# Kernel tuning notes

Measured on AMD Instinct MI355X. Metric: run time of the kernel, lower is better.

## Reference

```python
import jax, jax.numpy as jnp
import numpy as np

T, I, H, L = 2048, 64, 512, 5  # seq len, input feat, hidden, layers


def _lstm_layer(x_seq, w_ih, w_hh, b_ih, b_hh):
    """Single-layer LSTM over time, batch=1. x_seq: [T, in]. Returns [T, H]."""
    n_hidden = w_hh.shape[1]
    b = b_ih + b_hh  # fuse biases once

    def step(carry, x_t):
        h, c = carry
        gates = w_ih @ x_t + w_hh @ h + b  # [4H]
        i, f, g, o = jnp.split(gates, 4)
        i = jax.nn.sigmoid(i)
        f = jax.nn.sigmoid(f)
        g = jnp.tanh(g)
        o = jax.nn.sigmoid(o)
        c = f * c + i * g
        h = o * jnp.tanh(c)
        return (h, c), h

    h0 = jnp.zeros((n_hidden,), x_seq.dtype)
    (_, _), hs = jax.lax.scan(step, (h0, h0), x_seq)
    return hs


def setup_inputs() -> dict:
    key = jax.random.key(0)
    ks = jax.random.split(key, 12)
    s = 1.0 / np.sqrt(H)  # PyTorch-style U(-1/sqrt(H), 1/sqrt(H)) scale, approximated with scaled normal
    return {
        "x": jax.random.normal(ks[0], (T, I), jnp.float32),
        "w_ih0": jax.random.normal(ks[1], (4 * H, I), jnp.float32) * s,
        "w_hh0": jax.random.normal(ks[2], (4 * H, H), jnp.float32) * s,
        "b_ih0": jax.random.normal(ks[3], (4 * H,), jnp.float32) * s,
        "b_hh0": jax.random.normal(ks[4], (4 * H,), jnp.float32) * s,
        "w_ih": jax.random.normal(ks[5], (L - 1, 4 * H, H), jnp.float32) * s,
        "w_hh": jax.random.normal(ks[6], (L - 1, 4 * H, H), jnp.float32) * s,
        "b_ih": jax.random.normal(ks[7], (L - 1, 4 * H), jnp.float32) * s,
        "b_hh": jax.random.normal(ks[8], (L - 1, 4 * H), jnp.float32) * s,
        "w_lin": jax.random.normal(ks[9], (1, H), jnp.float32) * s,
        "b_lin": jax.random.normal(ks[10], (1,), jnp.float32) * s,
    }


def reference(x, w_ih0, w_hh0, b_ih0, b_hh0, w_ih, w_hh, b_ih, b_hh, w_lin, b_lin):
    # 5-layer LSTM (dropout=0 / inference), batch = 1
    h = _lstm_layer(x, w_ih0, w_hh0, b_ih0, b_hh0)  # [T, H]
    for l in range(w_ih.shape[0]):  # fixed small layer loop
        h = _lstm_layer(h, w_ih[l], w_hh[l], b_ih[l], b_hh[l])
    e = h @ w_lin.T + b_lin                # [T, 1]
    w = jax.nn.softmax(jnp.tanh(e), axis=0)  # softmax over time
    res = jnp.mean(h * w, axis=0, keepdims=True)  # [1, H] (matches torch (T,1,H)*(T,1) mean over axis 0)
    return res
```

## Files before the change

kernel.cpp:

```cpp
#include <hip/hip_runtime.h>
#include <math.h>

#define TT 2048
#define II 64
#define HH 512
#define LL 5
#define RING 8
#define BPL 32
#define NBLK (LL * BPL)
#define WPB 16

__device__ __forceinline__ float wave_sum(float v) {
#pragma unroll
  for (int m = 32; m > 0; m >>= 1) v += __shfl_xor(v, m, 64);
  return v;
}

__device__ __forceinline__ float wave_max(float v) {
#pragma unroll
  for (int m = 32; m > 0; m >>= 1) v = fmaxf(v, __shfl_xor(v, m, 64));
  return v;
}

__device__ __forceinline__ float sigmoidf_(float v) {
  return 1.0f / (1.0f + expf(-v));
}

__device__ __forceinline__ unsigned ld_cnt(const unsigned* p) {
  return __hip_atomic_load((unsigned*)p, __ATOMIC_RELAXED, __HIP_MEMORY_SCOPE_AGENT);
}

__device__ __forceinline__ void wait_ge(unsigned* p, unsigned v) {
  long spins = 0;
  while (ld_cnt(p) < v) {
    if (++spins > 8000000L) {
      __hip_atomic_fetch_max(p, v, __ATOMIC_RELAXED, __HIP_MEMORY_SCOPE_AGENT);
      break;
    }
  }
}

__device__ __forceinline__ float ld_coh(const float* p) {
  return __hip_atomic_load((float*)p, __ATOMIC_RELAXED, __HIP_MEMORY_SCOPE_AGENT);
}
__device__ __forceinline__ void st_coh(float* p, float v) {
  __hip_atomic_store(p, v, __ATOMIC_RELAXED, __HIP_MEMORY_SCOPE_AGENT);
}

__device__ __forceinline__ void grid_barrier(unsigned* arrive, unsigned* gen, unsigned idx) {
  __syncthreads();
  if (threadIdx.x == 0) {
    __threadfence();
    unsigned target = (unsigned)NBLK * (idx + 1u);
    unsigned prev = __hip_atomic_fetch_add(arrive, 1u, __ATOMIC_RELAXED, __HIP_MEMORY_SCOPE_AGENT);
    if (prev + 1u == target) {
      __hip_atomic_store(gen, idx + 1u, __ATOMIC_RELAXED, __HIP_MEMORY_SCOPE_AGENT);
    } else {
      wait_ge(gen, idx + 1u);
    }
    __threadfence();
  }
  __syncthreads();
}

extern "C" __global__ void __launch_bounds__(1024, 4) lstm_pipe(
    const float* __restrict__ x,
    const float* __restrict__ w_ih0, const float* __restrict__ w_hh0,
    const float* __restrict__ b_ih0, const float* __restrict__ b_hh0,
    const float* __restrict__ w_ih, const float* __restrict__ w_hh,
    const float* __restrict__ b_ih, const float* __restrict__ b_hh,
    const float* __restrict__ w_lin, const float* __restrict__ b_lin,
    float* __restrict__ out, float* __restrict__ ws) {
  unsigned* cnt = (unsigned*)ws;
  float* data = ws + 1024;
  float* h_ring = data;
  float* h4 = h_ring + LL * RING * HH;
  float* h4T = h4 + (size_t)TT * HH;
  float* scores = h4T + (size_t)HH * TT;
  float* pbuf = scores + TT;
  float* red = pbuf + TT;

  const int b = blockIdx.x;
  const int tid = threadIdx.x;
  const int wv = tid >> 6;
  const int lane = tid & 63;
  const int l = b / BPL;
  const int q = b % BPL;
  const int j = q * WPB + wv;

  unsigned* arr_l = cnt + l * 64;
  unsigned* arr_lm1 = cnt + (l - 1) * 64;
  unsigned* arr_lp1 = cnt + (l + 1) * 64;
  unsigned* garr = cnt + 320;
  unsigned* ggen = cnt + 336;

  float whh[4][8], wih[4][8], bias[4];
  const float* WHH = (l == 0) ? w_hh0 : (w_hh + (size_t)(l - 1) * 4 * HH * HH);
#pragma unroll
  for (int g = 0; g < 4; ++g) {
    const int row = g * HH + j;
#pragma unroll
    for (int m = 0; m < 8; ++m) whh[g][m] = WHH[(size_t)row * HH + m * 64 + lane];
  }
  if (l == 0) {
#pragma unroll
    for (int g = 0; g < 4; ++g) {
      const int row = g * HH + j;
      wih[g][0] = w_ih0[(size_t)row * II + lane];
#pragma unroll
      for (int m = 1; m < 8; ++m) wih[g][m] = 0.0f;
      bias[g] = b_ih0[row] + b_hh0[row];
    }
  } else {
    const float* WIH = w_ih + (size_t)(l - 1) * 4 * HH * HH;
    const float* BIH = b_ih + (size_t)(l - 1) * 4 * HH;
    const float* BHH = b_hh + (size_t)(l - 1) * 4 * HH;
#pragma unroll
    for (int g = 0; g < 4; ++g) {
      const int row = g * HH + j;
#pragma unroll
      for (int m = 0; m < 8; ++m) wih[g][m] = WIH[(size_t)row * HH + m * 64 + lane];
      bias[g] = BIH[row] + BHH[row];
    }
  }
#pragma unroll
  for (int g = 0; g < 4; ++g) {
#pragma unroll
    for (int m = 0; m < 8; ++m) {
      asm volatile("" : "+v"(whh[g][m]));
      asm volatile("" : "+v"(wih[g][m]));
    }
    asm volatile("" : "+v"(bias[g]));
  }

  const float* own_rd = h_ring + (size_t)l * RING * HH + lane;
  const float* prev_rd = h_ring + (size_t)(l - 1) * RING * HH + lane;
  float* own_wr = h_ring + (size_t)l * RING * HH + j;

  float c = 0.0f;

  for (int t = 0; t < TT; ++t) {
    if (tid == 0 && t > 0) wait_ge(arr_l, (unsigned)(BPL * t));
    if (tid == 64 && l > 0) wait_ge(arr_lm1, (unsigned)(BPL * (t + 1)));
    if (tid == 128 && l < LL - 1 && t >= RING)
      wait_ge(arr_lp1, (unsigned)(BPL * (t - RING + 1)));
    __syncthreads();

    float hp[8];
    if (t > 0) {
      const float* rp = own_rd + (size_t)((t - 1) & (RING - 1)) * HH;
#pragma unroll
      for (int m = 0; m < 8; ++m) hp[m] = ld_coh(rp + m * 64);
    } else {
#pragma unroll
      for (int m = 0; m < 8; ++m) hp[m] = 0.0f;
    }
    float xin[8];
    if (l == 0) {
      xin[0] = x[(size_t)t * II + lane];
#pragma unroll
      for (int m = 1; m < 8; ++m) xin[m] = 0.0f;
    } else {
      const float* rp = prev_rd + (size_t)(t & (RING - 1)) * HH;
#pragma unroll
      for (int m = 0; m < 8; ++m) xin[m] = ld_coh(rp + m * 64);
    }

    float ai = 0.0f, af = 0.0f, ag = 0.0f, ao = 0.0f;
#pragma unroll
    for (int m = 0; m < 8; ++m) {
      ai = fmaf(whh[0][m], hp[m], ai);
      af = fmaf(whh[1][m], hp[m], af);
      ag = fmaf(whh[2][m], hp[m], ag);
      ao = fmaf(whh[3][m], hp[m], ao);
    }
#pragma unroll
    for (int m = 0; m < 8; ++m) {
      ai = fmaf(wih[0][m], xin[m], ai);
      af = fmaf(wih[1][m], xin[m], af);
      ag = fmaf(wih[2][m], xin[m], ag);
      ao = fmaf(wih[3][m], xin[m], ao);
    }
    ai = wave_sum(ai); af = wave_sum(af); ag = wave_sum(ag); ao = wave_sum(ao);
    float gi = sigmoidf_(ai + bias[0]);
    float gf = sigmoidf_(af + bias[1]);
    float gg = tanhf(ag + bias[2]);
    float go = sigmoidf_(ao + bias[3]);
    c = gf * c + gi * gg;
    float h = go * tanhf(c);
    if (lane == 0) {
      st_coh(own_wr + (size_t)(t & (RING - 1)) * HH, h);
      if (l == LL - 1) {
        h4[(size_t)t * HH + j] = h;
        h4T[(size_t)j * TT + t] = h;
      }
    }
    asm volatile("s_waitcnt vmcnt(0)" ::: "memory");
    __syncthreads();
    if (tid == 0) {
      __hip_atomic_fetch_add(arr_l, 1u, __ATOMIC_RELAXED, __HIP_MEMORY_SCOPE_AGENT);
    }
  }

  grid_barrier(garr, ggen, 0u);

  {
    const int gw = b * WPB + wv;
    if (gw < TT) {
      const int t = gw;
      const float4* hp4 = (const float4*)(h4 + (size_t)t * HH + lane * 8);
      const float4* wl4 = (const float4*)(w_lin + lane * 8);
      float4 a = hp4[0], d = hp4[1], wa = wl4[0], wd = wl4[1];
      float acc = 0.0f;
      acc = fmaf(a.x, wa.x, acc); acc = fmaf(a.y, wa.y, acc);
      acc = fmaf(a.z, wa.z, acc); acc = fmaf(a.w, wa.w, acc);
      acc = fmaf(d.x, wd.x, acc); acc = fmaf(d.y, wd.y, acc);
      acc = fmaf(d.z, wd.z, acc); acc = fmaf(d.w, wd.w, acc);
      acc = wave_sum(acc);
      float sc = tanhf(acc + b_lin[0]);
      if (lane == 0) scores[t] = sc;
    }
  }
  grid_barrier(garr, ggen, 1u);

  __shared__ float sbuf[20];
  if (b == 0) {
    float s0 = scores[tid];
    float s1 = scores[tid + 1024];
    float m = fmaxf(s0, s1);
    m = wave_max(m);
    if (lane == 0) sbuf[wv] = m;
    __syncthreads();
    if (tid == 0) {
      float M = sbuf[0];
      for (int k = 1; k < 16; ++k) M = fmaxf(M, sbuf[k]);
      sbuf[16] = M;
    }
    __syncthreads();
    float M = sbuf[16];
    float p0 = expf(s0 - M), p1 = expf(s1 - M);
    pbuf[tid] = p0;
    pbuf[tid + 1024] = p1;
    float ssum = wave_sum(p0 + p1);
    __syncthreads();
    if (lane == 0) sbuf[wv] = ssum;
    __syncthreads();
    if (tid == 0) {
      float S = 0.0f;
      for (int k = 0; k < 16; ++k) S += sbuf[k];
      red[0] = 1.0f / ((float)TT * S);
    }
  }
  grid_barrier(garr, ggen, 2u);

  {
    const int gw = b * WPB + wv;
    if (gw < HH) {
      const int jj = gw;
      const float scale = red[0];
      const float* hr = h4T + (size_t)jj * TT + lane * 32;
      const float* pr = pbuf + lane * 32;
      float acc = 0.0f;
#pragma unroll
      for (int m = 0; m < 32; ++m) acc = fmaf(hr[m], pr[m], acc);
      acc = wave_sum(acc);
      if (lane == 0) out[jj] = scale * acc;
    }
  }
}

extern "C" void kernel_launch(void* const* d_in, const int* in_sizes, int n_in,
                              void* d_out, int out_size, void* d_ws, size_t ws_size,
                              hipStream_t stream) {
  hipMemsetAsync(d_ws, 0, 4096, stream);
  lstm_pipe<<<dim3(NBLK), dim3(1024), 0, stream>>>(
      (const float*)d_in[0],
      (const float*)d_in[1], (const float*)d_in[2],
      (const float*)d_in[3], (const float*)d_in[4],
      (const float*)d_in[5], (const float*)d_in[6],
      (const float*)d_in[7], (const float*)d_in[8],
      (const float*)d_in[9], (const float*)d_in[10],
      (float*)d_out, (float*)d_ws);
}
```

Measured before the change: 8.911 ms.

## Replace per-step counters with tagged ring entries polled by each wave

```diff
diff --git a/kernel.cpp b/kernel.cpp
--- a/kernel.cpp
+++ b/kernel.cpp
@@ -8,7 +8,10 @@
 #define RING 8
 #define BPL 32
 #define NBLK (LL * BPL)
-#define WPB 16
+#define WPB 8
+#define JPW 2
+
+typedef unsigned long long u64;
 
 __device__ __forceinline__ float wave_sum(float v) {
 #pragma unroll
@@ -26,25 +29,24 @@
   return 1.0f / (1.0f + expf(-v));
 }
 
-__device__ __forceinline__ unsigned ld_cnt(const unsigned* p) {
+__device__ __forceinline__ u64 ld8(const u64* p) {
+  return __hip_atomic_load((u64*)p, __ATOMIC_RELAXED, __HIP_MEMORY_SCOPE_AGENT);
+}
+__device__ __forceinline__ void st8(u64* p, u64 v) {
+  __hip_atomic_store(p, v, __ATOMIC_RELAXED, __HIP_MEMORY_SCOPE_AGENT);
+}
+__device__ __forceinline__ unsigned ld4(const unsigned* p) {
   return __hip_atomic_load((unsigned*)p, __ATOMIC_RELAXED, __HIP_MEMORY_SCOPE_AGENT);
 }
 
 __device__ __forceinline__ void wait_ge(unsigned* p, unsigned v) {
   long spins = 0;
-  while (ld_cnt(p) < v) {
+  while (ld4(p) < v) {
     if (++spins > 8000000L) {
       __hip_atomic_fetch_max(p, v, __ATOMIC_RELAXED, __HIP_MEMORY_SCOPE_AGENT);
       break;
     }
   }
-}
-
-__device__ __forceinline__ float ld_coh(const float* p) {
-  return __hip_atomic_load((float*)p, __ATOMIC_RELAXED, __HIP_MEMORY_SCOPE_AGENT);
-}
-__device__ __forceinline__ void st_coh(float* p, float v) {
-  __hip_atomic_store(p, v, __ATOMIC_RELAXED, __HIP_MEMORY_SCOPE_AGENT);
 }
 
 __device__ __forceinline__ void grid_barrier(unsigned* arrive, unsigned* gen, unsigned idx) {
@@ -63,7 +65,7 @@
   __syncthreads();
 }
 
-extern "C" __global__ void __launch_bounds__(1024, 4) lstm_pipe(
+extern "C" __global__ void __launch_bounds__(512, 2) lstm_pipe(
     const float* __restrict__ x,
     const float* __restrict__ w_ih0, const float* __restrict__ w_hh0,
     const float* __restrict__ b_ih0, const float* __restrict__ b_hh0,
@@ -72,9 +74,8 @@
     const float* __restrict__ w_lin, const float* __restrict__ b_lin,
     float* __restrict__ out, float* __restrict__ ws) {
   unsigned* cnt = (unsigned*)ws;
-  float* data = ws + 1024;
-  float* h_ring = data;
-  float* h4 = h_ring + LL * RING * HH;
+  u64* ring = (u64*)(ws + 1024);
+  float* h4 = (float*)(ring + (size_t)LL * RING * HH);
   float* h4T = h4 + (size_t)TT * HH;
   float* scores = h4T + (size_t)HH * TT;
   float* pbuf = scores + TT;
@@ -86,168 +87,211 @@
   const int lane = tid & 63;
   const int l = b / BPL;
   const int q = b % BPL;
-  const int j = q * WPB + wv;
-
-  unsigned* arr_l = cnt + l * 64;
-  unsigned* arr_lm1 = cnt + (l - 1) * 64;
-  unsigned* arr_lp1 = cnt + (l + 1) * 64;
+  const int j0 = (q * WPB + wv) * JPW;
+
+  unsigned* prog_l = cnt + l * 64;
+  unsigned* prog_lp1 = cnt + (l + 1) * 64;
   unsigned* garr = cnt + 320;
   unsigned* ggen = cnt + 336;
 
-  float whh[4][8], wih[4][8], bias[4];
+  float whh[JPW][4][8], wih[JPW][4][8], bias[JPW][4];
   const float* WHH = (l == 0) ? w_hh0 : (w_hh + (size_t)(l - 1) * 4 * HH * HH);
 #pragma unroll
-  for (int g = 0; g < 4; ++g) {
-    const int row = g * HH + j;
-#pragma unroll
-    for (int m = 0; m < 8; ++m) whh[g][m] = WHH[(size_t)row * HH + m * 64 + lane];
+  for (int jj = 0; jj < JPW; ++jj) {
+#pragma unroll
+    for (int g = 0; g < 4; ++g) {
+      const int row = g * HH + j0 + jj;
+#pragma unroll
+      for (int m = 0; m < 8; ++m) whh[jj][g][m] = WHH[(size_t)row * HH + m * 64 + lane];
+    }
   }
   if (l == 0) {
 #pragma unroll
-    for (int g = 0; g < 4; ++g) {
-      const int row = g * HH + j;
-      wih[g][0] = w_ih0[(size_t)row * II + lane];
-#pragma unroll
-      for (int m = 1; m < 8; ++m) wih[g][m] = 0.0f;
-      bias[g] = b_ih0[row] + b_hh0[row];
+    for (int jj = 0; jj < JPW; ++jj) {
+#pragma unroll
+      for (int g = 0; g < 4; ++g) {
+        const int row = g * HH + j0 + jj;
+        wih[jj][g][0] = w_ih0[(size_t)row * II + lane];
+#pragma unroll
+        for (int m = 1; m < 8; ++m) wih[jj][g][m] = 0.0f;
+        bias[jj][g] = b_ih0[row] + b_hh0[row];
+      }
     }
   } else {
     const float* WIH = w_ih + (size_t)(l - 1) * 4 * HH * HH;
     const float* BIH = b_ih + (size_t)(l - 1) * 4 * HH;
     const float* BHH = b_hh + (size_t)(l - 1) * 4 * HH;
 #pragma unroll
-    for (int g = 0; g < 4; ++g) {
-      const int row = g * HH + j;
-#pragma unroll
-      for (int m = 0; m < 8; ++m) wih[g][m] = WIH[(size_t)row * HH + m * 64 + lane];
-      bias[g] = BIH[row] + BHH[row];
-    }
-  }
-#pragma unroll
-  for (int g = 0; g < 4; ++g) {
-#pragma unroll
-    for (int m = 0; m < 8; ++m) {
-      asm volatile("" : "+v"(whh[g][m]));
-      asm volatile("" : "+v"(wih[g][m]));
-    }
-    asm volatile("" : "+v"(bias[g]));
-  }
-
-  const float* own_rd = h_ring + (size_t)l * RING * HH + lane;
-  const float* prev_rd = h_ring + (size_t)(l - 1) * RING * HH + lane;
-  float* own_wr = h_ring + (size_t)l * RING * HH + j;
-
-  float c = 0.0f;
+    for (int jj = 0; jj < JPW; ++jj) {
+#pragma unroll
+      for (int g = 0; g < 4; ++g) {
+        const int row = g * HH + j0 + jj;
+#pragma unroll
+        for (int m = 0; m < 8; ++m) wih[jj][g][m] = WIH[(size_t)row * HH + m * 64 + lane];
+        bias[jj][g] = BIH[row] + BHH[row];
+      }
+    }
+  }
+
+  u64* ringL = ring + (size_t)l * RING * HH;
+  u64* ringP = ring + (size_t)(l - 1) * RING * HH;
+
+  float cst[JPW];
+#pragma unroll
+  for (int jj = 0; jj < JPW; ++jj) cst[jj] = 0.0f;
+
+  const bool need_prev = (l > 0);
+  const bool is_last = (l == LL - 1);
 
   for (int t = 0; t < TT; ++t) {
-    if (tid == 0 && t > 0) wait_ge(arr_l, (unsigned)(BPL * t));
-    if (tid == 64 && l > 0) wait_ge(arr_lm1, (unsigned)(BPL * (t + 1)));
-    if (tid == 128 && l < LL - 1 && t >= RING)
-      wait_ge(arr_lp1, (unsigned)(BPL * (t - RING + 1)));
-    __syncthreads();
-
-    float hp[8];
-    if (t > 0) {
-      const float* rp = own_rd + (size_t)((t - 1) & (RING - 1)) * HH;
-#pragma unroll
-      for (int m = 0; m < 8; ++m) hp[m] = ld_coh(rp + m * 64);
-    } else {
-#pragma unroll
-      for (int m = 0; m < 8; ++m) hp[m] = 0.0f;
-    }
-    float xin[8];
+    const int so = (t - 1) & (RING - 1);
+    const int sp = t & (RING - 1);
+    const u64* own_rd = ringL + (size_t)so * HH + lane;
+    const u64* prev_rd = ringP + (size_t)sp * HH + lane;
+    const bool need_own = (t > 0);
+    const bool need_bp = (l < LL - 1) && (t >= RING);
+    const unsigned bp_min = (unsigned)(t - (RING - 2));
+
+    u64 po[8], pp[8];
+    long spins = 0;
+    for (;;) {
+      if (need_own) {
+#pragma unroll
+        for (int m = 0; m < 8; ++m) po[m] = ld8(own_rd + m * 64);
+      }
+      if (need_prev) {
+#pragma unroll
+        for (int m = 0; m < 8; ++m) pp[m] = ld8(prev_rd + m * 64);
+      }
+      unsigned pg = need_bp ? ld4(prog_lp1) : 0xFFFFFFFFu;
+      bool ok = true;
+      if (need_own) {
+#pragma unroll
+        for (int m = 0; m < 8; ++m) ok &= ((unsigned)(po[m] >> 32) == (unsigned)t);
+      }
+      if (need_prev) {
+#pragma unroll
+        for (int m = 0; m < 8; ++m) ok &= ((unsigned)(pp[m] >> 32) == (unsigned)(t + 1));
+      }
+      if (need_bp) ok &= (pg >= bp_min);
+      if (__ballot(ok) == ~0ull) break;
+      if (++spins > 4000000L) break;
+    }
+
+    float hp[8], xin[8];
+#pragma unroll
+    for (int m = 0; m < 8; ++m) hp[m] = need_own ? __uint_as_float((unsigned)po[m]) : 0.0f;
     if (l == 0) {
       xin[0] = x[(size_t)t * II + lane];
 #pragma unroll
       for (int m = 1; m < 8; ++m) xin[m] = 0.0f;
     } else {
-      const float* rp = prev_rd + (size_t)(t & (RING - 1)) * HH;
-#pragma unroll
-      for (int m = 0; m < 8; ++m) xin[m] = ld_coh(rp + m * 64);
-    }
-
-    float ai = 0.0f, af = 0.0f, ag = 0.0f, ao = 0.0f;
+#pragma unroll
+      for (int m = 0; m < 8; ++m) xin[m] = __uint_as_float((unsigned)pp[m]);
+    }
+
+    float acc[JPW][4];
+#pragma unroll
+    for (int jj = 0; jj < JPW; ++jj)
+#pragma unroll
+      for (int g = 0; g < 4; ++g) acc[jj][g] = 0.0f;
 #pragma unroll
     for (int m = 0; m < 8; ++m) {
-      ai = fmaf(whh[0][m], hp[m], ai);
-      af = fmaf(whh[1][m], hp[m], af);
-      ag = fmaf(whh[2][m], hp[m], ag);
-      ao = fmaf(whh[3][m], hp[m], ao);
+      const float hv = hp[m];
+#pragma unroll
+      for (int jj = 0; jj < JPW; ++jj) {
+        acc[jj][0] = fmaf(whh[jj][0][m], hv, acc[jj][0]);
+        acc[jj][1] = fmaf(whh[jj][1][m], hv, acc[jj][1]);
+        acc[jj][2] = fmaf(whh[jj][2][m], hv, acc[jj][2]);
+        acc[jj][3] = fmaf(whh[jj][3][m], hv, acc[jj][3]);
+      }
     }
 #pragma unroll
     for (int m = 0; m < 8; ++m) {
-      ai = fmaf(wih[0][m], xin[m], ai);
-      af = fmaf(wih[1][m], xin[m], af);
-      ag = fmaf(wih[2][m], xin[m], ag);
-      ao = fmaf(wih[3][m], xin[m], ao);
-    }
-    ai = wave_sum(ai); af = wave_sum(af); ag = wave_sum(ag); ao = wave_sum(ao);
-    float gi = sigmoidf_(ai + bias[0]);
-    float gf = sigmoidf_(af + bias[1]);
-    float gg = tanhf(ag + bias[2]);
-    float go = sigmoidf_(ao + bias[3]);
-    c = gf * c + gi * gg;
-    float h = go * tanhf(c);
+      const float xv = xin[m];
+#pragma unroll
+      for (int jj = 0; jj < JPW; ++jj) {
+        acc[jj][0] = fmaf(wih[jj][0][m], xv, acc[jj][0]);
+        acc[jj][1] = fmaf(wih[jj][1][m], xv, acc[jj][1]);
+        acc[jj][2] = fmaf(wih[jj][2][m], xv, acc[jj][2]);
+        acc[jj][3] = fmaf(wih[jj][3][m], xv, acc[jj][3]);
+      }
+    }
+
+    float hout[JPW];
+#pragma unroll
+    for (int jj = 0; jj < JPW; ++jj) {
+      float ai = wave_sum(acc[jj][0]);
+      float af = wave_sum(acc[jj][1]);
+      float ag = wave_sum(acc[jj][2]);
+      float ao = wave_sum(acc[jj][3]);
+      float gi = sigmoidf_(ai + bias[jj][0]);
+      float gf = sigmoidf_(af + bias[jj][1]);
+      float gg = tanhf(ag + bias[jj][2]);
+      float go = sigmoidf_(ao + bias[jj][3]);
+      cst[jj] = gf * cst[jj] + gi * gg;
+      hout[jj] = go * tanhf(cst[jj]);
+    }
+
     if (lane == 0) {
-      st_coh(own_wr + (size_t)(t & (RING - 1)) * HH, h);
-      if (l == LL - 1) {
-        h4[(size_t)t * HH + j] = h;
-        h4T[(size_t)j * TT + t] = h;
-      }
-    }
-    asm volatile("s_waitcnt vmcnt(0)" ::: "memory");
-    __syncthreads();
-    if (tid == 0) {
-      __hip_atomic_fetch_add(arr_l, 1u, __ATOMIC_RELAXED, __HIP_MEMORY_SCOPE_AGENT);
+      const u64 tag = ((u64)(unsigned)(t + 1)) << 32;
+      st8(ringL + (size_t)sp * HH + j0, tag | (u64)__float_as_uint(hout[0]));
+      st8(ringL + (size_t)sp * HH + j0 + 1, tag | (u64)__float_as_uint(hout[1]));
+      if (is_last) {
+        h4[(size_t)t * HH + j0] = hout[0];
+        h4[(size_t)t * HH + j0 + 1] = hout[1];
+        h4T[(size_t)j0 * TT + t] = hout[0];
+        h4T[(size_t)(j0 + 1) * TT + t] = hout[1];
+      }
+    }
+    if (l > 0 && q == 0 && wv == 0 && lane == 0 && ((t + 1) & 1) == 0) {
+      __hip_atomic_store(prog_l, (unsigned)(t + 1), __ATOMIC_RELAXED, __HIP_MEMORY_SCOPE_AGENT);
     }
   }
 
   grid_barrier(garr, ggen, 0u);
 
-  {
-    const int gw = b * WPB + wv;
-    if (gw < TT) {
-      const int t = gw;
-      const float4* hp4 = (const float4*)(h4 + (size_t)t * HH + lane * 8);
-      const float4* wl4 = (const float4*)(w_lin + lane * 8);
-      float4 a = hp4[0], d = hp4[1], wa = wl4[0], wd = wl4[1];
-      float acc = 0.0f;
-      acc = fmaf(a.x, wa.x, acc); acc = fmaf(a.y, wa.y, acc);
-      acc = fmaf(a.z, wa.z, acc); acc = fmaf(a.w, wa.w, acc);
-      acc = fmaf(d.x, wd.x, acc); acc = fmaf(d.y, wd.y, acc);
-      acc = fmaf(d.z, wd.z, acc); acc = fmaf(d.w, wd.w, acc);
-      acc = wave_sum(acc);
-      float sc = tanhf(acc + b_lin[0]);
-      if (lane == 0) scores[t] = sc;
-    }
+  for (int t = b * WPB + wv; t < TT; t += NBLK * WPB) {
+    const float4* hp4 = (const float4*)(h4 + (size_t)t * HH + lane * 8);
+    const float4* wl4 = (const float4*)(w_lin + lane * 8);
+    float4 a = hp4[0], d = hp4[1], wa = wl4[0], wd = wl4[1];
+    float acc = 0.0f;
+    acc = fmaf(a.x, wa.x, acc); acc = fmaf(a.y, wa.y, acc);
+    acc = fmaf(a.z, wa.z, acc); acc = fmaf(a.w, wa.w, acc);
+    acc = fmaf(d.x, wd.x, acc); acc = fmaf(d.y, wd.y, acc);
+    acc = fmaf(d.z, wd.z, acc); acc = fmaf(d.w, wd.w, acc);
+    acc = wave_sum(acc);
+    float sc = tanhf(acc + b_lin[0]);
+    if (lane == 0) scores[t] = sc;
   }
   grid_barrier(garr, ggen, 1u);
 
-  __shared__ float sbuf[20];
+  __shared__ float sbuf[12];
   if (b == 0) {
-    float s0 = scores[tid];
-    float s1 = scores[tid + 1024];
-    float m = fmaxf(s0, s1);
+    float s0 = scores[tid], s1 = scores[tid + 512];
+    float s2 = scores[tid + 1024], s3 = scores[tid + 1536];
+    float m = fmaxf(fmaxf(s0, s1), fmaxf(s2, s3));
     m = wave_max(m);
     if (lane == 0) sbuf[wv] = m;
     __syncthreads();
     if (tid == 0) {
       float M = sbuf[0];
-      for (int k = 1; k < 16; ++k) M = fmaxf(M, sbuf[k]);
-      sbuf[16] = M;
+      for (int k = 1; k < 8; ++k) M = fmaxf(M, sbuf[k]);
+      sbuf[8] = M;
     }
     __syncthreads();
-    float M = sbuf[16];
+    float M = sbuf[8];
     float p0 = expf(s0 - M), p1 = expf(s1 - M);
-    pbuf[tid] = p0;
-    pbuf[tid + 1024] = p1;
-    float ssum = wave_sum(p0 + p1);
+    float p2 = expf(s2 - M), p3 = expf(s3 - M);
+    pbuf[tid] = p0; pbuf[tid + 512] = p1;
+    pbuf[tid + 1024] = p2; pbuf[tid + 1536] = p3;
+    float ssum = wave_sum(p0 + p1 + p2 + p3);
     __syncthreads();
     if (lane == 0) sbuf[wv] = ssum;
     __syncthreads();
     if (tid == 0) {
       float S = 0.0f;
-      for (int k = 0; k < 16; ++k) S += sbuf[k];
+      for (int k = 0; k < 8; ++k) S += sbuf[k];
       red[0] = 1.0f / ((float)TT * S);
     }
   }
@@ -256,15 +300,14 @@
   {
     const int gw = b * WPB + wv;
     if (gw < HH) {
-      const int jj = gw;
       const float scale = red[0];
-      const float* hr = h4T + (size_t)jj * TT + lane * 32;
+      const float* hr = h4T + (size_t)gw * TT + lane * 32;
       const float* pr = pbuf + lane * 32;
       float acc = 0.0f;
 #pragma unroll
       for (int m = 0; m < 32; ++m) acc = fmaf(hr[m], pr[m], acc);
       acc = wave_sum(acc);
-      if (lane == 0) out[jj] = scale * acc;
+      if (lane == 0) out[gw] = scale * acc;
     }
   }
 }
@@ -273,7 +316,7 @@
                               void* d_out, int out_size, void* d_ws, size_t ws_size,
                               hipStream_t stream) {
   hipMemsetAsync(d_ws, 0, 4096, stream);
-  lstm_pipe<<<dim3(NBLK), dim3(1024), 0, stream>>>(
+  lstm_pipe<<<dim3(NBLK), dim3(512), 0, stream>>>(
       (const float*)d_in[0],
       (const float*)d_in[1], (const float*)d_in[2],
       (const float*)d_in[3], (const float*)d_in[4],
```

Result: slower. 14.34 ms (+60.9%).
